# Optimization experiments

Measured on AMD Instinct MI355X. Metric: run time of the kernel, lower is better.

The kernel has to match this reference:

```python
import jax, jax.numpy as jnp
import numpy as np
from math import sqrt

B, CIN, COUT, H, W = 32, 64, 64, 64, 64
CH = CIN // 2  # chunked half-channels fed to each branch
NORM_SCALE = 0.5
EPS = 1e-5


def conv2d(x, w, pad):
    # x: [B,C,H,W], w: [O,I,kh,kw]
    return jax.lax.conv_general_dilated(
        x, w, (1, 1), [(pad, pad), (pad, pad)],
        dimension_numbers=('NCHW', 'OIHW', 'NCHW'))


def unfold(x, k, stride=1, pad=0):
    # torch nn.Unfold: [B,C,H,W] -> [B, C*k*k, L], feature order (C, kh, kw)
    if pad:
        x = jnp.pad(x, ((0, 0), (0, 0), (pad, pad), (pad, pad)))
    b, c, h, w = x.shape
    oh = (h - k) // stride + 1
    ow = (w - k) // stride + 1
    cols = jnp.stack([
        x[:, :, i:i + (oh - 1) * stride + 1:stride, j:j + (ow - 1) * stride + 1:stride]
        for i in range(k) for j in range(k)], axis=2)  # [b,c,k*k,oh,ow]
    return cols.reshape(b, c * k * k, oh * ow)


def batchnorm(x):
    # training-mode BatchNorm2d, affine=False, biased variance, eps=1e-5
    m = x.mean(axis=(0, 2, 3), keepdims=True)
    v = x.var(axis=(0, 2, 3), keepdims=True)
    return (x - m) * jax.lax.rsqrt(v + EPS)


def attn_kernel(x, w1, w2, k, use_softmax):
    # AttnConvKernel.forward -> [B, Cout, Cin, k*k]
    b, cin = x.shape[0], x.shape[1]
    cout = w2.shape[0]
    y1 = unfold(conv2d(x, w1, 1), k, stride=k)  # [b, cin*k*k, L]
    y2 = unfold(conv2d(x, w2, 1), k, stride=k)  # [b, cout*k*k, L]
    L = y1.shape[-1]
    y1 = y1.reshape(b, cin, k * k, L)
    y2 = y2.reshape(b, cout, k * k, L)
    a = jnp.einsum('bikl,bokl->boik', y1, y2) / sqrt(cin * k * k)
    if use_softmax:
        a = jax.nn.softmax(a.reshape(b, cout, cin * k * k), axis=2)
        a = a.reshape(b, cout, cin, k * k)
    return a


def branch(x, wk1c1, wk1c2, wk2c1, wk2c2, wconv, aw, a_pre, a_post):
    # ResBatchNorm2d(shortcut=0.01) -> AttnConv2d -> ResBatchNorm2d(shortcut=0.6)
    h = NORM_SCALE * batchnorm(x) + 0.01 * a_pre * x
    k1 = attn_kernel(h, wk1c1, wk1c2, 3, False)   # [B,Cout,Ch,9]
    k2 = attn_kernel(h, wk2c1, wk2c2, 1, True)    # [B,Cout,Ch,1]
    ak = k2 * (k1 + aw)                           # broadcast over k*k
    b, cout = ak.shape[0], ak.shape[1]
    u = unfold(conv2d(h, wconv, 1), 3, 1, 1)      # [B, Ch*9, H*W]
    v = jnp.einsum('bok,bkl->bol', ak.reshape(b, cout, -1), u)
    v = v.reshape(b, cout, H, W)
    return NORM_SCALE * batchnorm(v) + 0.6 * a_post * v


def setup_inputs() -> dict:
    key = jax.random.key(0)
    ks = jax.random.split(key, 8)
    s = 0.05
    return {
        'x': jax.random.normal(ks[0], (B, CIN, H, W), jnp.float32),
        'wk1c1': jax.random.normal(ks[1], (4, CH, CH, 3, 3), jnp.float32) * s,
        'wk1c2': jax.random.normal(ks[2], (4, COUT, CH, 3, 3), jnp.float32) * s,
        'wk2c1': jax.random.normal(ks[3], (4, CH, CH, 3, 3), jnp.float32) * s,
        'wk2c2': jax.random.normal(ks[4], (4, COUT, CH, 3, 3), jnp.float32) * s,
        'wconv': jax.random.normal(ks[5], (4, CH, CH, 3, 3), jnp.float32) * s,
        'attn_w': jax.random.normal(ks[6], (4, COUT, CH, 9), jnp.float32) * s,
        'a_pre': jnp.ones((4,), jnp.float32),
        'a_post': jnp.ones((4,), jnp.float32),
        'conv_momentum': jnp.float32(1.0),
    }


def reference(x, wk1c1, wk1c2, wk2c1, wk2c2, wconv, attn_w, a_pre, a_post, conv_momentum):
    x1, x2 = jnp.split(x, 2, axis=1)
    xs = (x1, x2, x1, x2)
    ys = [branch(xs[i], wk1c1[i], wk1c2[i], wk2c1[i], wk2c2[i], wconv[i],
                 attn_w[i], a_pre[i], a_post[i]) for i in range(4)]
    y = (ys[0] + ys[1] + ys[2] * ys[3]) / sqrt(3.0)
    # in_channels == out_channels -> scalar conv_momentum path; feature_map_stack identity (num_heads=1)
    return 0.99 * conv_momentum * x + y
```

## Files before the change

kernel.cpp:

```cpp
#include <hip/hip_runtime.h>
#include <math.h>

#define HW 4096
#define EPSV 1e-5f

typedef _Float16 half8 __attribute__((ext_vector_type(8)));
typedef float f32x4 __attribute__((ext_vector_type(4)));
union H8 { half8 v; ushort4 q[2]; uint4 u4; };

#define SLAB_F 23068672ull
#define OFF_Y1A 0
#define OFF_Y2A 2097152
#define OFF_Y1B 4194304
#define OFF_Y2B 8388608
#define OFF_CCB 12582912
#define OFF_P1  14680064
#define OFF_P2  18874368

__global__ __launch_bounds__(256) void bn_partial_kernel(
    const float* __restrict__ x, float* __restrict__ pstat) {
  int c = blockIdx.x, b = blockIdx.y;
  int tid = threadIdx.x;
  const float4* p = (const float4*)(x + ((size_t)b * 64 + c) * HW);
  float sm = 0.f, s2 = 0.f;
  #pragma unroll
  for (int i = 0; i < 4; i++) {
    float4 v = p[tid + i * 256];
    sm += v.x + v.y + v.z + v.w;
    s2 += v.x * v.x + v.y * v.y + v.z * v.z + v.w * v.w;
  }
  __shared__ float sh[2][256];
  sh[0][tid] = sm; sh[1][tid] = s2;
  __syncthreads();
  for (int off = 128; off > 0; off >>= 1) {
    if (tid < off) { sh[0][tid] += sh[0][tid + off]; sh[1][tid] += sh[1][tid + off]; }
    __syncthreads();
  }
  if (tid == 0) {
    pstat[((size_t)b * 64 + c) * 2] = sh[0][0];
    pstat[((size_t)b * 64 + c) * 2 + 1] = sh[1][0];
  }
}

__global__ __launch_bounds__(256) void bnv_partial_kernel(
    const _Float16* __restrict__ vb0, size_t vstrideH, float* __restrict__ pstat) {
  int c = blockIdx.x, b = blockIdx.y, br = blockIdx.z;
  int tid = threadIdx.x;
  const _Float16* row = vb0 + (size_t)br * vstrideH + ((size_t)b * 64 + c) * HW;
  float sm = 0.f, s2 = 0.f;
  #pragma unroll
  for (int i = 0; i < 2; i++) {
    H8 v; v.u4 = *(const uint4*)(row + (tid + i * 256) * 8);
    #pragma unroll
    for (int k = 0; k < 8; k++) { float t = (float)v.v[k]; sm += t; s2 += t * t; }
  }
  __shared__ float sh[2][256];
  sh[0][tid] = sm; sh[1][tid] = s2;
  __syncthreads();
  for (int off = 128; off > 0; off >>= 1) {
    if (tid < off) { sh[0][tid] += sh[0][tid + off]; sh[1][tid] += sh[1][tid + off]; }
    __syncthreads();
  }
  if (tid == 0) {
    pstat[(((size_t)br * 32 + b) * 64 + c) * 2] = sh[0][0];
    pstat[(((size_t)br * 32 + b) * 64 + c) * 2 + 1] = sh[1][0];
  }
}

__global__ __launch_bounds__(256) void pack_static_kernel(
    const float* __restrict__ wk1c1, const float* __restrict__ wk1c2,
    const float* __restrict__ wk2c1, const float* __restrict__ wk2c2,
    const float* __restrict__ wconv, _Float16* __restrict__ wpk) {
  int idx = blockIdx.x * 256 + threadIdx.x;
  int j = idx & 7, lane = (idx >> 3) & 63;
  int tap = (idx >> 9) % 9;
  int chunk = (idx / 4608) % 14;
  int br = idx / 64512;
  int g = lane >> 4;
  int c = (j < 4) ? 4 * g + j : 16 + 4 * g + (j - 4);
  const float* src; int ol0;
  if (chunk < 2)       { src = wk1c1 + (size_t)br * 32 * 288; ol0 = chunk * 16; }
  else if (chunk < 6)  { src = wk1c2 + (size_t)br * 64 * 288; ol0 = (chunk - 2) * 16; }
  else if (chunk < 8)  { src = wk2c1 + (size_t)br * 32 * 288; ol0 = (chunk - 6) * 16; }
  else if (chunk < 12) { src = wk2c2 + (size_t)br * 64 * 288; ol0 = (chunk - 8) * 16; }
  else                 { src = wconv + (size_t)br * 32 * 288; ol0 = (chunk - 12) * 16; }
  int o = ol0 + (lane & 15);
  wpk[idx] = (_Float16)(src[((size_t)o * 32 + c) * 9 + tap]);
}

template <int MODE>
__global__ __launch_bounds__(256) void conv_mfma_kernel(
    const float* __restrict__ xin, const _Float16* __restrict__ wAll,
    const float* __restrict__ pstat, const float* __restrict__ a_pre,
    int brBase, float* __restrict__ slabBase, size_t slabStride,
    _Float16* __restrict__ vb0, size_t vstrideH) {
  const int NCHUNK = (MODE == 0) ? 14 : 4;
  int bz = blockIdx.z;
  int br = brBase + bz;
  float* slab = slabBase + (size_t)bz * slabStride;
  __shared__ _Float16 hsh[6 * 66 * 36];
  __shared__ float alsh[32], besh[32];
  int tid = threadIdx.x;
  int b = blockIdx.y, r0 = blockIdx.x * 4;
  int ch0 = (br & 1) * 32;
  if (MODE == 0 && tid < 32) {
    float s = 0.f, s2 = 0.f;
    for (int bb = 0; bb < 32; bb++) {
      size_t p = ((size_t)bb * 64 + ch0 + tid) * 2;
      s += pstat[p]; s2 += pstat[p + 1];
    }
    const float N = 131072.f;
    float m = s / N;
    float r = rsqrtf(s2 / N - m * m + EPSV);
    alsh[tid] = 0.5f * r + 0.01f * a_pre[br];
    besh[tid] = -0.5f * m * r;
  }
  __syncthreads();
  for (int t = tid; t < 384; t += 256) {
    int row = t >> 6, colh = ((t & 63) >> 5) ? 65 : 0, c = t & 31;
    hsh[(row * 66 + colh) * 36 + c] = (_Float16)0.f;
  }
  if (MODE == 0) {
    for (int t = tid; t < 32 * 96; t += 256) {
      int c = t / 96, p4 = (t % 96) * 4;
      int row = p4 >> 6, col = p4 & 63;
      int rg = r0 + row - 1;
      float4 v4 = {0.f, 0.f, 0.f, 0.f};
      if ((unsigned)rg < 64u)
        v4 = *(const float4*)&xin[((size_t)b * 64 + ch0 + c) * HW + (rg << 6) + col];
      float a = alsh[c], be = besh[c];
      _Float16* dst = &hsh[((size_t)row * 66 + col + 1) * 36 + c];
      dst[0]   = (_Float16)(v4.x * a + be);
      dst[36]  = (_Float16)(v4.y * a + be);
      dst[72]  = (_Float16)(v4.z * a + be);
      dst[108] = (_Float16)(v4.w * a + be);
    }
  } else {
    const _Float16* cin = (const _Float16*)(slab + OFF_CCB);
    for (int t = tid; t < 32 * 48; t += 256) {
      int c = t / 48, p8 = (t % 48) * 8;
      int row = p8 >> 6, col = p8 & 63;
      int rg = r0 + row - 1;
      H8 v; v.u4 = make_uint4(0, 0, 0, 0);
      if ((unsigned)rg < 64u)
        v.u4 = *(const uint4*)&cin[((size_t)b * 32 + c) * HW + (rg << 6) + col];
      _Float16* dst = &hsh[((size_t)row * 66 + col + 1) * 36 + c];
      #pragma unroll
      for (int k = 0; k < 8; k++) dst[36 * k] = v.v[k];
    }
  }
  __syncthreads();
  int w = tid >> 6, l = tid & 63;
  int ln = l & 15, g = l >> 4;
  H8 bfr[4][9];
  #pragma unroll
  for (int pf = 0; pf < 4; pf++)
    #pragma unroll
    for (int dyi = 0; dyi < 3; dyi++)
      #pragma unroll
      for (int dxi = 0; dxi < 3; dxi++) {
        const _Float16* p = &hsh[(((size_t)(w + dyi)) * 66 + pf * 16 + ln + dxi) * 36 + 4 * g];
        H8 f;
        f.q[0] = *(const ushort4*)p;
        f.q[1] = *(const ushort4*)(p + 16);
        bfr[pf][dyi * 3 + dxi] = f;
      }
  const _Float16* wb = (MODE == 0)
      ? wAll + (size_t)br * 64512
      : wAll + (size_t)br * 589824 + (size_t)b * 18432;
  for (int chunk = 0; chunk < NCHUNK; chunk++) {
    H8 af[9];
    #pragma unroll
    for (int t = 0; t < 9; t++)
      af[t].u4 = *(const uint4*)(wb + (((size_t)chunk * 9 + t) * 64 + l) * 8);
    _Float16* ob; int Cb, ol0;
    if (MODE == 0) {
      if (chunk < 2)       { ob = (_Float16*)(slab + OFF_Y1A); Cb = 32; ol0 = chunk * 16; }
      else if (chunk < 6)  { ob = (_Float16*)(slab + OFF_Y1B); Cb = 64; ol0 = (chunk - 2) * 16; }
      else if (chunk < 8)  { ob = (_Float16*)(slab + OFF_Y2A); Cb = 32; ol0 = (chunk - 6) * 16; }
      else if (chunk < 12) { ob = (_Float16*)(slab + OFF_Y2B); Cb = 64; ol0 = (chunk - 8) * 16; }
      else                 { ob = (_Float16*)(slab + OFF_CCB); Cb = 32; ol0 = (chunk - 12) * 16; }
    } else { ob = vb0 + (size_t)br * vstrideH; Cb = 64; ol0 = chunk * 16; }
    #pragma unroll
    for (int pf = 0; pf < 4; pf++) {
      f32x4 acc = {0.f, 0.f, 0.f, 0.f};
      #pragma unroll
      for (int t = 0; t < 9; t++)
        acc = __builtin_amdgcn_mfma_f32_16x16x32_f16(bfr[pf][t].v, af[t].v, acc, 0, 0, 0);
      union { _Float16 h[4]; ushort4 u; } sv;
      #pragma unroll
      for (int j = 0; j < 4; j++) sv.h[j] = (_Float16)acc[j];
      int px = ((r0 + w) << 6) + pf * 16 + 4 * g;
      *(ushort4*)&ob[((size_t)b * Cb + ol0 + ln) * HW + px] = sv.u;
    }
  }
}

__global__ __launch_bounds__(256) void attn1_mfma_kernel(
    float* __restrict__ slabBase, size_t slabStride) {
  __shared__ _Float16 comp[3][96][34];
  int rg = blockIdx.x, b = blockIdx.y;
  float* slab = slabBase + (size_t)blockIdx.z * slabStride;
  const _Float16* y1 = (const _Float16*)(slab + OFF_Y1A);
  const _Float16* y2 = (const _Float16*)(slab + OFF_Y1B);
  int tid = threadIdx.x;
  for (int t = tid; t < 4896; t += 256) ((unsigned int*)comp)[t] = 0u;
  int w = tid >> 6, lr = tid & 15, g = (tid >> 4) & 3;
  f32x4 acc[9][2];
  #pragma unroll
  for (int kk = 0; kk < 9; kk++) {
    acc[kk][0] = (f32x4){0.f, 0.f, 0.f, 0.f};
    acc[kk][1] = (f32x4){0.f, 0.f, 0.f, 0.f};
  }
  for (int tri = 0; tri < 3; tri++) {
    #pragma unroll
    for (int ri = 0; ri < 3; ri++) {
      int r = rg * 9 + tri * 3 + ri;
      __syncthreads();
      for (int t = tid; t < 288; t += 256) {
        int ch = t / 3, oct = t % 3;
        const _Float16* src =
            (ch < 32 ? y1 + ((size_t)b * 32 + ch) * HW
                     : y2 + ((size_t)b * 64 + (ch - 32)) * HW) + (r << 6) + oct * 24;
        union { uint4 q[3]; ushort u[24]; } dat;
        dat.q[0] = *(const uint4*)(src);
        dat.q[1] = *(const uint4*)(src + 8);
        dat.q[2] = *(const uint4*)(src + 16);
        #pragma unroll
        for (int dj = 0; dj < 3; dj++) {
          union { ushort u[8]; uint4 q; } o_;
          #pragma unroll
          for (int m = 0; m < 8; m++) o_.u[m] = dat.u[dj + 3 * m];
          if (oct == 2) { o_.u[5] = 0; o_.u[6] = 0; o_.u[7] = 0; }
          *(uint4*)&comp[dj][ch][oct * 8] = o_.q;
        }
      }
      __syncthreads();
      #pragma unroll
      for (int dj = 0; dj < 3; dj++) {
        H8 af, bf0, bf1;
        const _Float16* pa = &comp[dj][32 + 16 * w + lr][4 * g];
        af.q[0] = *(const ushort4*)pa;  af.q[1] = *(const ushort4*)(pa + 16);
        const _Float16* p0 = &comp[dj][lr][4 * g];
        bf0.q[0] = *(const ushort4*)p0; bf0.q[1] = *(const ushort4*)(p0 + 16);
        const _Float16* p1 = &comp[dj][16 + lr][4 * g];
        bf1.q[0] = *(const ushort4*)p1; bf1.q[1] = *(const ushort4*)(p1 + 16);
        acc[ri * 3 + dj][0] =
            __builtin_amdgcn_mfma_f32_16x16x32_f16(af.v, bf0.v, acc[ri * 3 + dj][0], 0, 0, 0);
        acc[ri * 3 + dj][1] =
            __builtin_amdgcn_mfma_f32_16x16x32_f16(af.v, bf1.v, acc[ri * 3 + dj][1], 0, 0, 0);
      }
    }
  }
  float* part = slab + OFF_P1;
  #pragma unroll
  for (int kk = 0; kk < 9; kk++) {
    size_t base = (((size_t)rg * 32 + b) * 9 + kk) * 2048 + (16 * w + 4 * g) * 32 + lr;
    #pragma unroll
    for (int j = 0; j < 4; j++) {
      part[base + (size_t)j * 32] = acc[kk][0][j];
      part[base + (size_t)j * 32 + 16] = acc[kk][1][j];
    }
  }
}

__global__ __launch_bounds__(256) void attn2_mfma_kernel(
    float* __restrict__ slabBase, size_t slabStride) {
  __shared__ _Float16 comp[96][68];
  int ps = blockIdx.x, b = blockIdx.y;
  float* slab = slabBase + (size_t)blockIdx.z * slabStride;
  const _Float16* y1 = (const _Float16*)(slab + OFF_Y2A);
  const _Float16* y2 = (const _Float16*)(slab + OFF_Y2B);
  int tid = threadIdx.x;
  int w = tid >> 6, lr = tid & 15, g = (tid >> 4) & 3;
  f32x4 acc0 = {0.f, 0.f, 0.f, 0.f}, acc1 = {0.f, 0.f, 0.f, 0.f};
  for (int st = 0; st < 8; st++) {
    __syncthreads();
    #pragma unroll
    for (int t0 = 0; t0 < 3; t0++) {
      int t = tid + t0 * 256;
      int ch = t >> 3, part = t & 7;
      const _Float16* src =
          (ch < 32 ? y1 + ((size_t)b * 32 + ch) * HW
                   : y2 + ((size_t)b * 64 + (ch - 32)) * HW) + ps * 512 + st * 64 + part * 8;
      *(uint4*)&comp[ch][part * 8] = *(const uint4*)src;
    }
    __syncthreads();
    #pragma unroll
    for (int kh = 0; kh < 2; kh++) {
      H8 af, bf0, bf1;
      const _Float16* pa = &comp[32 + 16 * w + lr][kh * 32 + 4 * g];
      af.q[0] = *(const ushort4*)pa;  af.q[1] = *(const ushort4*)(pa + 16);
      const _Float16* p0 = &comp[lr][kh * 32 + 4 * g];
      bf0.q[0] = *(const ushort4*)p0; bf0.q[1] = *(const ushort4*)(p0 + 16);
      const _Float16* p1 = &comp[16 + lr][kh * 32 + 4 * g];
      bf1.q[0] = *(const ushort4*)p1; bf1.q[1] = *(const ushort4*)(p1 + 16);
      acc0 = __builtin_amdgcn_mfma_f32_16x16x32_f16(af.v, bf0.v, acc0, 0, 0, 0);
      acc1 = __builtin_amdgcn_mfma_f32_16x16x32_f16(af.v, bf1.v, acc1, 0, 0, 0);
    }
  }
  float* p2 = slab + OFF_P2;
  size_t base = ((size_t)ps * 32 + b) * 2048 + (16 * w + 4 * g) * 32 + lr;
  #pragma unroll
  for (int j = 0; j < 4; j++) {
    p2[base + (size_t)j * 32] = acc0[j];
    p2[base + (size_t)j * 32 + 16] = acc1[j];
  }
}

__global__ __launch_bounds__(320) void fused_ak_kernel(
    float* __restrict__ slabBase, size_t slabStride, int brBase,
    const float* __restrict__ aw, _Float16* __restrict__ wdynB) {
  int o = blockIdx.x, b = blockIdx.y;
  int bz = blockIdx.z, br = brBase + bz;
  float* slab = slabBase + (size_t)bz * slabStride;
  const float* part1 = slab + OFF_P1;
  const float* part2 = slab + OFF_P2;
  const float* awb = aw + (size_t)br * 18432;
  _Float16* wdyn = wdynB + (size_t)br * 589824;
  int tid = threadIdx.x;
  __shared__ float sm[33];
  if (tid < 32) {
    float s = 0.f;
    #pragma unroll
    for (int ps = 0; ps < 8; ps++) s += part2[((size_t)ps * 32 + b) * 2048 + o * 32 + tid];
    sm[tid] = s * 0.17677669529663687f;
  }
  __syncthreads();
  if (tid == 0) {
    float mx = -1e30f;
    for (int k = 0; k < 32; k++) mx = fmaxf(mx, sm[k]);
    float sum = 0.f;
    for (int k = 0; k < 32; k++) { float e = expf(sm[k] - mx); sm[k] = e; sum += e; }
    sm[32] = 1.0f / sum;
  }
  __syncthreads();
  if (tid < 288) {
    int i = tid / 9, kk = tid % 9;
    float a1v = 0.f;
    #pragma unroll
    for (int rg = 0; rg < 7; rg++)
      a1v += part1[(((size_t)rg * 32 + b) * 9 + kk) * 2048 + o * 32 + i];
    a1v *= 0.05892556509887896f;
    float akv = sm[i] * sm[32] * (a1v + awb[(size_t)(o * 32 + i) * 9 + kk]);
    int chunk = o >> 4;
    int g = (i & 15) >> 2;
    int j = (i & 3) + ((i >= 16) ? 4 : 0);
    int lane = (g << 4) | (o & 15);
    wdyn[((((size_t)b * 4 + chunk) * 9 + kk) * 64 + lane) * 8 + j] = (_Float16)akv;
  }
}

__global__ __launch_bounds__(256) void finalize_kernel(
    const _Float16* __restrict__ vb0, size_t vstrideH,
    const float* __restrict__ pstat, const float* __restrict__ a_post,
    const float* __restrict__ x, const float* __restrict__ cm,
    float* __restrict__ out) {
  __shared__ float sga[256], sgb[256];
  int t = threadIdx.x;
  {
    int br = t >> 6, o = t & 63;
    float s = 0.f, s2 = 0.f;
    for (int bb = 0; bb < 32; bb++) {
      size_t p = (((size_t)br * 32 + bb) * 64 + o) * 2;
      s += pstat[p]; s2 += pstat[p + 1];
    }
    const float N = 131072.f;
    float m = s / N;
    float r = rsqrtf(s2 / N - m * m + EPSV);
    sga[t] = 0.5f * r + 0.6f * a_post[br];
    sgb[t] = -0.5f * m * r;
  }
  __syncthreads();
  size_t g8 = ((size_t)blockIdx.x * 256 + threadIdx.x) * 8;
  int o = (int)((g8 >> 12) & 63);
  float acc[8], ysv[8];
  #pragma unroll
  for (int br = 0; br < 4; br++) {
    float ga = sga[br * 64 + o], gb = sgb[br * 64 + o];
    H8 v; v.u4 = *(const uint4*)(vb0 + (size_t)br * vstrideH + g8);
    #pragma unroll
    for (int j = 0; j < 8; j++) {
      float y = ga * (float)v.v[j] + gb;
      if (br == 0) acc[j] = y;
      else if (br == 1) acc[j] += y;
      else if (br == 2) ysv[j] = y;
      else acc[j] += ysv[j] * y;
    }
  }
  float cmv = 0.99f * cm[0];
  const float4* xp = (const float4*)(x + g8);
  float4 x0 = xp[0], x1 = xp[1];
  float4 o0, o1;
  o0.x = cmv * x0.x + acc[0] * 0.5773502691896258f;
  o0.y = cmv * x0.y + acc[1] * 0.5773502691896258f;
  o0.z = cmv * x0.z + acc[2] * 0.5773502691896258f;
  o0.w = cmv * x0.w + acc[3] * 0.5773502691896258f;
  o1.x = cmv * x1.x + acc[4] * 0.5773502691896258f;
  o1.y = cmv * x1.y + acc[5] * 0.5773502691896258f;
  o1.z = cmv * x1.z + acc[6] * 0.5773502691896258f;
  o1.w = cmv * x1.w + acc[7] * 0.5773502691896258f;
  float4* op = (float4*)(out + g8);
  op[0] = o0;
  op[1] = o1;
}

extern "C" void kernel_launch(void* const* d_in, const int* in_sizes, int n_in,
                              void* d_out, int out_size, void* d_ws, size_t ws_size,
                              hipStream_t stream) {
  const float* x      = (const float*)d_in[0];
  const float* wk1c1  = (const float*)d_in[1];
  const float* wk1c2  = (const float*)d_in[2];
  const float* wk2c1  = (const float*)d_in[3];
  const float* wk2c2  = (const float*)d_in[4];
  const float* wconv  = (const float*)d_in[5];
  const float* attn_w = (const float*)d_in[6];
  const float* a_pre  = (const float*)d_in[7];
  const float* a_post = (const float*)d_in[8];
  const float* cm     = (const float*)d_in[9];
  float* out = (float*)d_out;

  const size_t FIX_F = 129024ull + 1179648ull + 16384ull;
  const size_t needB = (4 * SLAB_F + FIX_F) * 4;
  bool batched = ws_size >= needB;
  size_t nslab = batched ? 4 : 1;

  float* ws = (float*)d_ws;
  float* slab0 = ws;
  float* fixF  = ws + nslab * SLAB_F;
  _Float16* wpk   = (_Float16*)fixF;
  _Float16* wdynB = (_Float16*)(fixF + 129024);
  float* pstat    = fixF + 129024 + 1179648;
  _Float16* vb0;
  size_t vstrideH;
  if (batched) { vb0 = (_Float16*)(slab0 + OFF_P1); vstrideH = SLAB_F * 2; }
  else         { vb0 = (_Float16*)(fixF + FIX_F);   vstrideH = 8388608; }

  size_t SS = batched ? SLAB_F : 0;

  bn_partial_kernel<<<dim3(64, 32), 256, 0, stream>>>(x, pstat);
  pack_static_kernel<<<1008, 256, 0, stream>>>(wk1c1, wk1c2, wk2c1, wk2c2, wconv, wpk);

  if (batched) {
    conv_mfma_kernel<0><<<dim3(16, 32, 4), 256, 0, stream>>>(
        x, wpk, pstat, a_pre, 0, slab0, SS, nullptr, 0);
    attn1_mfma_kernel<<<dim3(7, 32, 4), 256, 0, stream>>>(slab0, SS);
    attn2_mfma_kernel<<<dim3(8, 32, 4), 256, 0, stream>>>(slab0, SS);
    fused_ak_kernel<<<dim3(64, 32, 4), 320, 0, stream>>>(slab0, SS, 0, attn_w, wdynB);
    conv_mfma_kernel<1><<<dim3(16, 32, 4), 256, 0, stream>>>(
        nullptr, wdynB, nullptr, nullptr, 0, slab0, SS, vb0, vstrideH);
  } else {
    for (int br = 0; br < 4; br++) {
      conv_mfma_kernel<0><<<dim3(16, 32, 1), 256, 0, stream>>>(
          x, wpk, pstat, a_pre, br, slab0, 0, nullptr, 0);
      attn1_mfma_kernel<<<dim3(7, 32, 1), 256, 0, stream>>>(slab0, 0);
      attn2_mfma_kernel<<<dim3(8, 32, 1), 256, 0, stream>>>(slab0, 0);
      fused_ak_kernel<<<dim3(64, 32, 1), 320, 0, stream>>>(slab0, 0, br, attn_w, wdynB);
      conv_mfma_kernel<1><<<dim3(16, 32, 1), 256, 0, stream>>>(
          nullptr, wdynB, nullptr, nullptr, br, slab0, 0, vb0, vstrideH);
    }
  }

  bnv_partial_kernel<<<dim3(64, 32, 4), 256, 0, stream>>>(vb0, vstrideH, pstat);
  finalize_kernel<<<4096, 256, 0, stream>>>(vb0, vstrideH, pstat, a_post, x, cm, out);
}
```

Before: 440.7 us.

## Process branches in pairs with a dedicated V buffer to shrink workspace footprint

Replaces the all-four-branches-batched path with a loop over branch pairs (two slabs at once), and moves the fp16 V output into a separate fixed buffer instead of inside each slab. This shrinks the workspace footprint, likely to keep intermediates more cache-resident (e.g. in MI355X's large last-level cache) or to let the batched path run when the workspace is smaller. The trade is twice as many kernel launches and less parallelism per launch than the four-branch batch. Kernels must correctly handle branch offset b0 together with blockIdx.z.

```diff
diff --git a/kernel.cpp b/kernel.cpp
--- a/kernel.cpp
+++ b/kernel.cpp
@@ -420,47 +420,34 @@
   const float* cm     = (const float*)d_in[9];
   float* out = (float*)d_out;
 
-  const size_t FIX_F = 129024ull + 1179648ull + 16384ull;
-  const size_t needB = (4 * SLAB_F + FIX_F) * 4;
-  bool batched = ws_size >= needB;
-  size_t nslab = batched ? 4 : 1;
+  const size_t VBUF_F = 16777216ull;
+  const size_t FIX_F  = 129024ull + 1179648ull + 16384ull;
+  size_t wsF = ws_size / 4;
+  int nslab = (wsF >= 2 * SLAB_F + FIX_F + VBUF_F) ? 2 : 1;
 
   float* ws = (float*)d_ws;
   float* slab0 = ws;
-  float* fixF  = ws + nslab * SLAB_F;
+  float* fixF  = ws + (size_t)nslab * SLAB_F;
   _Float16* wpk   = (_Float16*)fixF;
   _Float16* wdynB = (_Float16*)(fixF + 129024);
   float* pstat    = fixF + 129024 + 1179648;
-  _Float16* vb0;
-  size_t vstrideH;
-  if (batched) { vb0 = (_Float16*)(slab0 + OFF_P1); vstrideH = SLAB_F * 2; }
-  else         { vb0 = (_Float16*)(fixF + FIX_F);   vstrideH = 8388608; }
-
-  size_t SS = batched ? SLAB_F : 0;
+  _Float16* vb0   = (_Float16*)(fixF + FIX_F);
+  const size_t VSH = 8388608ull;
 
   bn_partial_kernel<<<dim3(64, 32), 256, 0, stream>>>(x, pstat);
   pack_static_kernel<<<1008, 256, 0, stream>>>(wk1c1, wk1c2, wk2c1, wk2c2, wconv, wpk);
 
-  if (batched) {
-    conv_mfma_kernel<0><<<dim3(16, 32, 4), 256, 0, stream>>>(
-        x, wpk, pstat, a_pre, 0, slab0, SS, nullptr, 0);
-    attn1_mfma_kernel<<<dim3(7, 32, 4), 256, 0, stream>>>(slab0, SS);
-    attn2_mfma_kernel<<<dim3(8, 32, 4), 256, 0, stream>>>(slab0, SS);
-    fused_ak_kernel<<<dim3(64, 32, 4), 320, 0, stream>>>(slab0, SS, 0, attn_w, wdynB);
-    conv_mfma_kernel<1><<<dim3(16, 32, 4), 256, 0, stream>>>(
-        nullptr, wdynB, nullptr, nullptr, 0, slab0, SS, vb0, vstrideH);
-  } else {
-    for (int br = 0; br < 4; br++) {
-      conv_mfma_kernel<0><<<dim3(16, 32, 1), 256, 0, stream>>>(
-          x, wpk, pstat, a_pre, br, slab0, 0, nullptr, 0);
-      attn1_mfma_kernel<<<dim3(7, 32, 1), 256, 0, stream>>>(slab0, 0);
-      attn2_mfma_kernel<<<dim3(8, 32, 1), 256, 0, stream>>>(slab0, 0);
-      fused_ak_kernel<<<dim3(64, 32, 1), 320, 0, stream>>>(slab0, 0, br, attn_w, wdynB);
-      conv_mfma_kernel<1><<<dim3(16, 32, 1), 256, 0, stream>>>(
-          nullptr, wdynB, nullptr, nullptr, br, slab0, 0, vb0, vstrideH);
-    }
-  }
-
-  bnv_partial_kernel<<<dim3(64, 32, 4), 256, 0, stream>>>(vb0, vstrideH, pstat);
-  finalize_kernel<<<4096, 256, 0, stream>>>(vb0, vstrideH, pstat, a_post, x, cm, out);
-}
+  for (int b0 = 0; b0 < 4; b0 += nslab) {
+    conv_mfma_kernel<0><<<dim3(16, 32, nslab), 256, 0, stream>>>(
+        x, wpk, pstat, a_pre, b0, slab0, SLAB_F, nullptr, 0);
+    attn1_mfma_kernel<<<dim3(7, 32, nslab), 256, 0, stream>>>(slab0, SLAB_F);
+    attn2_mfma_kernel<<<dim3(8, 32, nslab), 256, 0, stream>>>(slab0, SLAB_F);
+    fused_ak_kernel<<<dim3(64, 32, nslab), 320, 0, stream>>>(
+        slab0, SLAB_F, b0, attn_w, wdynB);
+    conv_mfma_kernel<1><<<dim3(16, 32, nslab), 256, 0, stream>>>(
+        nullptr, wdynB, nullptr, nullptr, b0, slab0, SLAB_F, vb0, VSH);
+  }
+
+  bnv_partial_kernel<<<dim3(64, 32, 4), 256, 0, stream>>>(vb0, VSH, pstat);
+  finalize_kernel<<<4096, 256, 0, stream>>>(vb0, VSH, pstat, a_post, x, cm, out);
+}
```

Measured after the change: 373.2 us. 1.18x faster.
